# Kernel optimization log

Hardware: AMD Instinct MI355X
Metric: run time of the kernel (lower is better)

Reference implementation:

```python
import jax, jax.numpy as jnp
import numpy as np

B, S, D = 16, 2048, 64
SCALE = 1.0 / np.sqrt(np.float32(D))  # forward divides by sqrt(embedding_dim=64)


def setup_inputs() -> dict:
    key = jax.random.key(0)
    ks = jax.random.split(key, 7)
    return {
        "x": jax.random.normal(ks[0], (B, S, D), dtype=jnp.float32),
        "Wq": jax.random.normal(ks[1], (D, D), dtype=jnp.float32) * 0.02,
        "bq": jax.random.normal(ks[2], (D,), dtype=jnp.float32) * 0.02,
        "Wk": jax.random.normal(ks[3], (D, D), dtype=jnp.float32) * 0.02,
        "bk": jax.random.normal(ks[4], (D,), dtype=jnp.float32) * 0.02,
        "Wv": jax.random.normal(ks[5], (D, D), dtype=jnp.float32) * 0.02,
        "bv": jax.random.normal(ks[6], (D,), dtype=jnp.float32) * 0.02,
    }


def reference(x, Wq, bq, Wk, bk, Wv, bv):
    # Linear projections (weights stored [in, out], math-equivalent to nn.Linear)
    q = jnp.einsum("bsd,de->bse", x, Wq) + bq
    k = jnp.einsum("bsd,de->bse", x, Wk) + bk
    v = jnp.einsum("bsd,de->bse", x, Wv) + bv
    # Unfused scores: [B, S, S]
    scores = jnp.einsum("bqd,bkd->bqk", q, k) * jnp.float32(SCALE)
    causal = jnp.tril(jnp.ones((S, S), dtype=bool))  # mask[:S,:S]
    scores = jnp.where(causal, scores, jnp.float32(-jnp.inf))
    attn = jax.nn.softmax(scores, axis=-1)
    # dropout is identity in eval mode (reference baseline)
    out = jnp.einsum("bqk,bkd->bqd", attn, v)
    return out
```

## Files before the change

kernel.cpp:

```cpp
#include <hip/hip_runtime.h>

#define NB 16
#define SS 2048
#define DD 64

typedef __attribute__((ext_vector_type(8))) short short8;
typedef __attribute__((ext_vector_type(4))) float f32x4;

#define SCL2E 0.18033688011112042f

#define GLOAD_LDS(g, l) __builtin_amdgcn_global_load_lds( \
    (const __attribute__((address_space(1))) void*)(g),   \
    (__attribute__((address_space(3))) void*)(l), 16, 0, 0)

__device__ __forceinline__ short f2bf(float f) {
  union { float f; unsigned u; } v; v.f = f;
  unsigned r = (v.u + 0x7fffu + ((v.u >> 16) & 1u)) >> 16;
  return (short)r;
}

__device__ __forceinline__ unsigned cvtpk_bf16(float lo, float hi) {
  unsigned r;
  asm("v_cvt_pk_bf16_f32 %0, %1, %2" : "=v"(r) : "v"(lo), "v"(hi));
  return r;
}

__device__ __forceinline__ short8 load_a_frag_f32(const float* p) {
  float4 u = *(const float4*)p;
  float4 w = *(const float4*)(p + 4);
  short8 r;
  r[0] = f2bf(u.x); r[1] = f2bf(u.y); r[2] = f2bf(u.z); r[3] = f2bf(u.w);
  r[4] = f2bf(w.x); r[5] = f2bf(w.y); r[6] = f2bf(w.z); r[7] = f2bf(w.w);
  return r;
}

__global__ __launch_bounds__(768) void proj_kernel(
    const float* __restrict__ x,
    const float* __restrict__ Wq, const float* __restrict__ bq,
    const float* __restrict__ Wk, const float* __restrict__ bk,
    const float* __restrict__ Wv, const float* __restrict__ bv,
    ushort* __restrict__ qo, ushort* __restrict__ ko, ushort* __restrict__ vt)
{
  __shared__ __align__(16) ushort Wt[3][64][72];
  __shared__ __align__(16) ushort Vs[64][68];
  const int t = threadIdx.x;
#pragma unroll
  for (int i = 0; i < 4; ++i) {
    int idx = i * 3072 + t * 4;
    int m = idx >> 12, rem = idx & 4095;
    int kk = rem >> 6, n0 = rem & 63;
    const float* src = (m == 0 ? Wq : (m == 1 ? Wk : Wv));
    float4 w4 = *(const float4*)(src + rem);
    Wt[m][n0 + 0][kk] = (ushort)f2bf(w4.x);
    Wt[m][n0 + 1][kk] = (ushort)f2bf(w4.y);
    Wt[m][n0 + 2][kk] = (ushort)f2bf(w4.z);
    Wt[m][n0 + 3][kk] = (ushort)f2bf(w4.w);
  }
  __syncthreads();

  const int lane = t & 63, w = t >> 6;
  const int l15 = lane & 15, quad = lane >> 4;
  const int mm = w >> 2, rr = w & 3;
  const int g = blockIdx.x * 64 + rr * 16 + l15;

  short8 b0 = load_a_frag_f32(x + (size_t)g * 64 + quad * 8);
  short8 b1 = load_a_frag_f32(x + (size_t)g * 64 + 32 + quad * 8);

  const float* bp = (mm == 0 ? bq : (mm == 1 ? bk : bv));
  ushort* outp = (mm == 0 ? qo : ko);

#pragma unroll
  for (int nt = 0; nt < 4; ++nt) {
    const ushort* ap = &Wt[mm][nt * 16 + l15][quad * 8];
    short8 a0 = *(const short8*)ap;
    short8 a1 = *(const short8*)(ap + 32);
    f32x4 acc = {0.f, 0.f, 0.f, 0.f};
    acc = __builtin_amdgcn_mfma_f32_16x16x32_bf16(a0, b0, acc, 0, 0, 0);
    acc = __builtin_amdgcn_mfma_f32_16x16x32_bf16(a1, b1, acc, 0, 0, 0);
    float4 bb = *(const float4*)(bp + nt * 16 + quad * 4);
    uint2 pk;
    pk.x = cvtpk_bf16(acc[0] + bb.x, acc[1] + bb.y);
    pk.y = cvtpk_bf16(acc[2] + bb.z, acc[3] + bb.w);
    if (mm == 2) {
      *(uint2*)&Vs[rr * 16 + l15][nt * 16 + quad * 4] = pk;
    } else {
      int colb = (nt * 16 + quad * 4) * 2;
      if (mm == 1) colb ^= (g & 7) << 4;
      *(uint2*)((char*)outp + (size_t)g * 128 + colb) = pk;
    }
  }
  __syncthreads();
  if (t < 256) {
    const int batch = blockIdx.x >> 5;
    const int ktile = blockIdx.x & 31;
    const int d = t >> 2, j0 = (t & 3) * 16;
    ushort tmp[16];
#pragma unroll
    for (int j = 0; j < 16; ++j) tmp[j] = Vs[j0 + j][d];
    char* base = (char*)vt + ((size_t)batch * SS * DD + ktile * 4096) * 2 + d * 128;
    const int sw = (d & 7) << 4;
    const int bcol = ((j0 >> 5) << 6) + (((j0 >> 4) & 1) << 3);
#pragma unroll
    for (int jj = 0; jj < 4; ++jj)
      *(uint2*)(base + ((bcol + jj * 16) ^ sw)) = ((uint2*)tmp)[jj];
  }
}

template<bool MASKED>
__device__ __forceinline__ void attn32(
    const f32x4 (&c)[2], float& l_acc, f32x4 (&acc)[4],
    const short8 (&vf)[4], int keybase, int qabs, int quad)
{
  unsigned pk[4];
#pragma unroll
  for (int ct = 0; ct < 2; ++ct) {
    float pe[4];
#pragma unroll
    for (int r = 0; r < 4; ++r) {
      float p = __builtin_amdgcn_exp2f(c[ct][r] * SCL2E);
      if (MASKED && (keybase + ct * 16 + quad * 4 + r > qabs)) p = 0.f;
      pe[r] = p;
      l_acc += p;
    }
    pk[ct * 2 + 0] = cvtpk_bf16(pe[0], pe[1]);
    pk[ct * 2 + 1] = cvtpk_bf16(pe[2], pe[3]);
  }
  int4 w4;
  w4.x = (int)pk[0]; w4.y = (int)pk[1]; w4.z = (int)pk[2]; w4.w = (int)pk[3];
  short8 pa = *(short8*)&w4;
  __builtin_amdgcn_s_setprio(1);
#pragma unroll
  for (int nt = 0; nt < 4; ++nt)
    acc[nt] = __builtin_amdgcn_mfma_f32_16x16x32_bf16(pa, vf[nt], acc[nt], 0, 0, 0);
  __builtin_amdgcn_s_setprio(0);
}

__device__ __forceinline__ void stage_tile(
    char* lds, const ushort* kg, const ushort* vt,
    size_t bbyte, int kt, int seg, int lane)
{
  const char* src = (seg < 2)
      ? (const char*)kg + bbyte + (size_t)kt * 8192 + seg * 4096
      : (const char*)vt + bbyte + (size_t)kt * 8192 + (seg - 2) * 4096;
  char* dst = lds + seg * 4096;
#pragma unroll
  for (int i = 0; i < 4; ++i)
    GLOAD_LDS(src + i * 1024 + lane * 16, dst + i * 1024);
}

__global__ __launch_bounds__(256) void attn_kernel(
    const ushort* __restrict__ qg, const ushort* __restrict__ kg,
    const ushort* __restrict__ vt, float* __restrict__ out)
{
  __shared__ __align__(16) char KV[2][16384];

  const int t = threadIdx.x, bid = blockIdx.x;
  const int batch = (bid & 7) * 2 + ((bid >> 3) & 1);
  const int qt = 63 - (bid >> 4);
  const int q0 = qt * 32;
  const int lane = t & 63, w = t >> 6;
  const int l15 = lane & 15, quad = lane >> 4;
  const int h = w >> 1;
  const int qgi = w & 1;
  const int qrow0 = q0 + qgi * 16;
  const size_t bbase = (size_t)batch * SS * DD;
  const size_t bbyte = bbase * 2;

  const ushort* qp = qg + bbase + (size_t)(qrow0 + l15) * 64 + quad * 8;
  short8 a0 = *(const short8*)qp;
  short8 a1 = *(const short8*)(qp + 32);

  f32x4 acc[4];
  float l = 0.f;
#pragma unroll
  for (int nt = 0; nt < 4; ++nt) acc[nt] = (f32x4){0.f, 0.f, 0.f, 0.f};

  const int ktotal = ((q0 + 31) >> 6) + 1;
  const int qabs = qrow0 + l15;

  stage_tile(&KV[0][0], kg, vt, bbyte, 0, w, lane);
  __syncthreads();

  int cur = 0;
  for (int kt = 0; kt < ktotal; ++kt) {
    if (kt + 1 < ktotal)
      stage_tile(&KV[cur ^ 1][0], kg, vt, bbyte, kt + 1, w, lane);

    const char* Kb = &KV[cur][0];
    const char* Vb = &KV[cur][8192];
    short8 kf0[2], kf1[2], vf[4];
#pragma unroll
    for (int c2 = 0; c2 < 2; ++c2) {
      int row = (2 * h + c2) * 16 + l15;
      int sw = (row & 7) << 4;
      kf0[c2] = *(const short8*)(Kb + row * 128 + ((quad * 16) ^ sw));
      kf1[c2] = *(const short8*)(Kb + row * 128 + ((64 + quad * 16) ^ sw));
    }
#pragma unroll
    for (int nt = 0; nt < 4; ++nt) {
      int drow = nt * 16 + l15;
      int sv = (drow & 7) << 4;
      vf[nt] = *(const short8*)(Vb + drow * 128 + ((h * 64 + quad * 16) ^ sv));
    }

    f32x4 c[2];
    __builtin_amdgcn_s_setprio(1);
#pragma unroll
    for (int c2 = 0; c2 < 2; ++c2) {
      f32x4 z = {0.f, 0.f, 0.f, 0.f};
      c[c2] = __builtin_amdgcn_mfma_f32_16x16x32_bf16(kf0[c2], a0, z, 0, 0, 0);
      c[c2] = __builtin_amdgcn_mfma_f32_16x16x32_bf16(kf1[c2], a1, c[c2], 0, 0, 0);
    }
    __builtin_amdgcn_s_setprio(0);

    const int keybase = kt * 64 + h * 32;
    if (kt == ktotal - 1)
      attn32<true >(c, l, acc, vf, keybase, qabs, quad);
    else
      attn32<false>(c, l, acc, vf, keybase, qabs, quad);

    __syncthreads();
    cur ^= 1;
  }

  l += __shfl_xor(l, 16);
  l += __shfl_xor(l, 32);

  __syncthreads();

  float* S = (float*)&KV[0][qgi * 8192];
  if (h == 1) {
#pragma unroll
    for (int r = 0; r < 4; ++r)
#pragma unroll
      for (int nt = 0; nt < 4; ++nt)
        S[(quad * 4 + r) * 68 + nt * 16 + l15] = acc[nt][r];
    if (lane < 16) S[1088 + lane] = l;
  }
  __syncthreads();
  if (h == 0) {
    float lt = l + S[1088 + l15];
#pragma unroll
    for (int r = 0; r < 4; ++r) {
      float iv = 1.0f / __shfl(lt, quad * 4 + r);
      float* orow = out + bbase + (size_t)(qrow0 + quad * 4 + r) * 64 + l15;
#pragma unroll
      for (int nt = 0; nt < 4; ++nt)
        orow[nt * 16] = (acc[nt][r] + S[(quad * 4 + r) * 68 + nt * 16 + l15]) * iv;
    }
  }
}

extern "C" void kernel_launch(void* const* d_in, const int* in_sizes, int n_in,
                              void* d_out, int out_size, void* d_ws, size_t ws_size,
                              hipStream_t stream) {
  (void)in_sizes; (void)n_in; (void)out_size; (void)ws_size;
  const float* x  = (const float*)d_in[0];
  const float* Wq = (const float*)d_in[1];
  const float* bq = (const float*)d_in[2];
  const float* Wk = (const float*)d_in[3];
  const float* bk = (const float*)d_in[4];
  const float* Wv = (const float*)d_in[5];
  const float* bv = (const float*)d_in[6];
  float* out = (float*)d_out;

  ushort* qws = (ushort*)d_ws;
  ushort* kws = qws + (size_t)NB * SS * DD;
  ushort* vws = kws + (size_t)NB * SS * DD;

  proj_kernel<<<dim3(NB * SS / 64), dim3(768), 0, stream>>>(
      x, Wq, bq, Wk, bk, Wv, bv, qws, kws, vws);
  attn_kernel<<<dim3(NB * (SS / 32)), dim3(256), 0, stream>>>(
      qws, kws, vws, out);
}
```

Before: 99.86 us.

## Fuse projection and attention into one persistent kernel with grid barrier

Replaces the separate projection and attention launches with a single 512-block kernel. Each block first computes Q/K/V projections for 64 rows, then waits at a global atomic grid barrier. It then processes two causal query tiles, paired long and short (63-u and u), so every block gets roughly equal work. This removes the second kernel launch and the tail imbalance of causal tiles. In exchange it needs a memset, a spin barrier that assumes all 512 blocks are co-resident, and fewer threads doing the projection phase.

```diff
diff --git a/kernel.cpp b/kernel.cpp
--- a/kernel.cpp
+++ b/kernel.cpp
@@ -3,6 +3,7 @@
 #define NB 16
 #define SS 2048
 #define DD 64
+#define NBLK 512
 
 typedef __attribute__((ext_vector_type(8))) short short8;
 typedef __attribute__((ext_vector_type(4))) float f32x4;
@@ -32,78 +33,6 @@
   r[0] = f2bf(u.x); r[1] = f2bf(u.y); r[2] = f2bf(u.z); r[3] = f2bf(u.w);
   r[4] = f2bf(w.x); r[5] = f2bf(w.y); r[6] = f2bf(w.z); r[7] = f2bf(w.w);
   return r;
-}
-
-__global__ __launch_bounds__(768) void proj_kernel(
-    const float* __restrict__ x,
-    const float* __restrict__ Wq, const float* __restrict__ bq,
-    const float* __restrict__ Wk, const float* __restrict__ bk,
-    const float* __restrict__ Wv, const float* __restrict__ bv,
-    ushort* __restrict__ qo, ushort* __restrict__ ko, ushort* __restrict__ vt)
-{
-  __shared__ __align__(16) ushort Wt[3][64][72];
-  __shared__ __align__(16) ushort Vs[64][68];
-  const int t = threadIdx.x;
-#pragma unroll
-  for (int i = 0; i < 4; ++i) {
-    int idx = i * 3072 + t * 4;
-    int m = idx >> 12, rem = idx & 4095;
-    int kk = rem >> 6, n0 = rem & 63;
-    const float* src = (m == 0 ? Wq : (m == 1 ? Wk : Wv));
-    float4 w4 = *(const float4*)(src + rem);
-    Wt[m][n0 + 0][kk] = (ushort)f2bf(w4.x);
-    Wt[m][n0 + 1][kk] = (ushort)f2bf(w4.y);
-    Wt[m][n0 + 2][kk] = (ushort)f2bf(w4.z);
-    Wt[m][n0 + 3][kk] = (ushort)f2bf(w4.w);
-  }
-  __syncthreads();
-
-  const int lane = t & 63, w = t >> 6;
-  const int l15 = lane & 15, quad = lane >> 4;
-  const int mm = w >> 2, rr = w & 3;
-  const int g = blockIdx.x * 64 + rr * 16 + l15;
-
-  short8 b0 = load_a_frag_f32(x + (size_t)g * 64 + quad * 8);
-  short8 b1 = load_a_frag_f32(x + (size_t)g * 64 + 32 + quad * 8);
-
-  const float* bp = (mm == 0 ? bq : (mm == 1 ? bk : bv));
-  ushort* outp = (mm == 0 ? qo : ko);
-
-#pragma unroll
-  for (int nt = 0; nt < 4; ++nt) {
-    const ushort* ap = &Wt[mm][nt * 16 + l15][quad * 8];
-    short8 a0 = *(const short8*)ap;
-    short8 a1 = *(const short8*)(ap + 32);
-    f32x4 acc = {0.f, 0.f, 0.f, 0.f};
-    acc = __builtin_amdgcn_mfma_f32_16x16x32_bf16(a0, b0, acc, 0, 0, 0);
-    acc = __builtin_amdgcn_mfma_f32_16x16x32_bf16(a1, b1, acc, 0, 0, 0);
-    float4 bb = *(const float4*)(bp + nt * 16 + quad * 4);
-    uint2 pk;
-    pk.x = cvtpk_bf16(acc[0] + bb.x, acc[1] + bb.y);
-    pk.y = cvtpk_bf16(acc[2] + bb.z, acc[3] + bb.w);
-    if (mm == 2) {
-      *(uint2*)&Vs[rr * 16 + l15][nt * 16 + quad * 4] = pk;
-    } else {
-      int colb = (nt * 16 + quad * 4) * 2;
-      if (mm == 1) colb ^= (g & 7) << 4;
-      *(uint2*)((char*)outp + (size_t)g * 128 + colb) = pk;
-    }
-  }
-  __syncthreads();
-  if (t < 256) {
-    const int batch = blockIdx.x >> 5;
-    const int ktile = blockIdx.x & 31;
-    const int d = t >> 2, j0 = (t & 3) * 16;
-    ushort tmp[16];
-#pragma unroll
-    for (int j = 0; j < 16; ++j) tmp[j] = Vs[j0 + j][d];
-    char* base = (char*)vt + ((size_t)batch * SS * DD + ktile * 4096) * 2 + d * 128;
-    const int sw = (d & 7) << 4;
-    const int bcol = ((j0 >> 5) << 6) + (((j0 >> 4) & 1) << 3);
-#pragma unroll
-    for (int jj = 0; jj < 4; ++jj)
-      *(uint2*)(base + ((bcol + jj * 16) ^ sw)) = ((uint2*)tmp)[jj];
-  }
 }
 
 template<bool MASKED>
@@ -148,105 +77,205 @@
     GLOAD_LDS(src + i * 1024 + lane * 16, dst + i * 1024);
 }
 
-__global__ __launch_bounds__(256) void attn_kernel(
-    const ushort* __restrict__ qg, const ushort* __restrict__ kg,
-    const ushort* __restrict__ vt, float* __restrict__ out)
+template<int M>
+__device__ __forceinline__ void proj_unit(
+    ushort (*Wt)[64][72], ushort (*Vs)[68],
+    const short8& b0, const short8& b1, const float* bp,
+    ushort* outp, int g, int lrow, int l15, int quad)
 {
-  __shared__ __align__(16) char KV[2][16384];
+#pragma unroll
+  for (int nt = 0; nt < 4; ++nt) {
+    short8 a0 = *(const short8*)&Wt[M][nt * 16 + l15][quad * 8];
+    short8 a1 = *(const short8*)&Wt[M][nt * 16 + l15][32 + quad * 8];
+    f32x4 acc = {0.f, 0.f, 0.f, 0.f};
+    acc = __builtin_amdgcn_mfma_f32_16x16x32_bf16(a0, b0, acc, 0, 0, 0);
+    acc = __builtin_amdgcn_mfma_f32_16x16x32_bf16(a1, b1, acc, 0, 0, 0);
+    float4 bb = *(const float4*)(bp + nt * 16 + quad * 4);
+    uint2 pk;
+    pk.x = cvtpk_bf16(acc[0] + bb.x, acc[1] + bb.y);
+    pk.y = cvtpk_bf16(acc[2] + bb.z, acc[3] + bb.w);
+    if (M == 2) {
+      *(uint2*)&Vs[lrow][nt * 16 + quad * 4] = pk;
+    } else if (M == 1) {
+      int colb = ((nt * 16 + quad * 4) * 2) ^ ((g & 7) << 4);
+      *(uint2*)((char*)outp + (size_t)g * 128 + colb) = pk;
+    } else {
+      *(uint2*)(outp + (size_t)g * 64 + nt * 16 + quad * 4) = pk;
+    }
+  }
+}
+
+__global__ __launch_bounds__(256, 2) void fused_kernel(
+    const float* __restrict__ x,
+    const float* __restrict__ Wq, const float* __restrict__ bq,
+    const float* __restrict__ Wk, const float* __restrict__ bk,
+    const float* __restrict__ Wv, const float* __restrict__ bv,
+    ushort* __restrict__ qo, ushort* __restrict__ ko, ushort* __restrict__ vt,
+    float* __restrict__ out, unsigned* __restrict__ bar)
+{
+  __shared__ __align__(16) char SMEM[2][16384];
 
   const int t = threadIdx.x, bid = blockIdx.x;
-  const int batch = (bid & 7) * 2 + ((bid >> 3) & 1);
-  const int qt = 63 - (bid >> 4);
-  const int q0 = qt * 32;
   const int lane = t & 63, w = t >> 6;
   const int l15 = lane & 15, quad = lane >> 4;
-  const int h = w >> 1;
-  const int qgi = w & 1;
-  const int qrow0 = q0 + qgi * 16;
-  const size_t bbase = (size_t)batch * SS * DD;
-  const size_t bbyte = bbase * 2;
-
-  const ushort* qp = qg + bbase + (size_t)(qrow0 + l15) * 64 + quad * 8;
-  short8 a0 = *(const short8*)qp;
-  short8 a1 = *(const short8*)(qp + 32);
-
-  f32x4 acc[4];
-  float l = 0.f;
-#pragma unroll
-  for (int nt = 0; nt < 4; ++nt) acc[nt] = (f32x4){0.f, 0.f, 0.f, 0.f};
-
-  const int ktotal = ((q0 + 31) >> 6) + 1;
-  const int qabs = qrow0 + l15;
-
-  stage_tile(&KV[0][0], kg, vt, bbyte, 0, w, lane);
+
+  {
+    ushort (*Wt)[64][72] = (ushort(*)[64][72])&SMEM[0][0];
+    ushort (*Vs)[68] = (ushort(*)[68])(&SMEM[0][0] + 27648);
+
+    const float* Ws[3] = {Wq, Wk, Wv};
+#pragma unroll
+    for (int m = 0; m < 3; ++m)
+#pragma unroll
+      for (int i = 0; i < 4; ++i) {
+        int idx = i * 1024 + t * 4;
+        int kk = idx >> 6, n0 = idx & 63;
+        float4 w4 = *(const float4*)(Ws[m] + kk * 64 + n0);
+        Wt[m][n0 + 0][kk] = (ushort)f2bf(w4.x);
+        Wt[m][n0 + 1][kk] = (ushort)f2bf(w4.y);
+        Wt[m][n0 + 2][kk] = (ushort)f2bf(w4.z);
+        Wt[m][n0 + 3][kk] = (ushort)f2bf(w4.w);
+      }
+    __syncthreads();
+
+    const int rh = w & 1;
+    const int batch = bid >> 5, kt64 = bid & 31;
+
+    for (int rg = 0; rg < 2; ++rg) {
+      const int g = bid * 64 + rg * 32 + rh * 16 + l15;
+      short8 b0 = load_a_frag_f32(x + (size_t)g * 64 + quad * 8);
+      short8 b1 = load_a_frag_f32(x + (size_t)g * 64 + 32 + quad * 8);
+      const int lrow = rh * 16 + l15;
+
+      if (w < 2) {
+        proj_unit<0>(Wt, Vs, b0, b1, bq, qo, g, lrow, l15, quad);
+        proj_unit<2>(Wt, Vs, b0, b1, bv, qo, g, lrow, l15, quad);
+      } else {
+        proj_unit<1>(Wt, Vs, b0, b1, bk, ko, g, lrow, l15, quad);
+      }
+      __syncthreads();
+
+      if (t < 128) {
+        const int d = t & 63, ct = t >> 6;
+        ushort tmp[16];
+#pragma unroll
+        for (int j = 0; j < 16; ++j) tmp[j] = Vs[ct * 16 + j][d];
+        char* base = (char*)vt + ((size_t)batch * SS * DD + kt64 * 4096) * 2 + d * 128;
+        const int sw = (d & 7) << 4;
+#pragma unroll
+        for (int q4 = 0; q4 < 4; ++q4)
+          *(uint2*)(base + ((rg * 64 + q4 * 16 + ct * 8) ^ sw)) = ((uint2*)tmp)[q4];
+      }
+      __syncthreads();
+    }
+  }
+
+  __threadfence();
+  if (t == 0) {
+    __hip_atomic_fetch_add(bar, 1u, __ATOMIC_ACQ_REL, __HIP_MEMORY_SCOPE_AGENT);
+    while (__hip_atomic_load(bar, __ATOMIC_ACQUIRE, __HIP_MEMORY_SCOPE_AGENT) < NBLK)
+      __builtin_amdgcn_s_sleep(4);
+  }
   __syncthreads();
-
-  int cur = 0;
-  for (int kt = 0; kt < ktotal; ++kt) {
-    if (kt + 1 < ktotal)
-      stage_tile(&KV[cur ^ 1][0], kg, vt, bbyte, kt + 1, w, lane);
-
-    const char* Kb = &KV[cur][0];
-    const char* Vb = &KV[cur][8192];
-    short8 kf0[2], kf1[2], vf[4];
-#pragma unroll
-    for (int c2 = 0; c2 < 2; ++c2) {
-      int row = (2 * h + c2) * 16 + l15;
-      int sw = (row & 7) << 4;
-      kf0[c2] = *(const short8*)(Kb + row * 128 + ((quad * 16) ^ sw));
-      kf1[c2] = *(const short8*)(Kb + row * 128 + ((64 + quad * 16) ^ sw));
-    }
-#pragma unroll
-    for (int nt = 0; nt < 4; ++nt) {
-      int drow = nt * 16 + l15;
-      int sv = (drow & 7) << 4;
-      vf[nt] = *(const short8*)(Vb + drow * 128 + ((h * 64 + quad * 16) ^ sv));
-    }
-
-    f32x4 c[2];
-    __builtin_amdgcn_s_setprio(1);
-#pragma unroll
-    for (int c2 = 0; c2 < 2; ++c2) {
-      f32x4 z = {0.f, 0.f, 0.f, 0.f};
-      c[c2] = __builtin_amdgcn_mfma_f32_16x16x32_bf16(kf0[c2], a0, z, 0, 0, 0);
-      c[c2] = __builtin_amdgcn_mfma_f32_16x16x32_bf16(kf1[c2], a1, c[c2], 0, 0, 0);
-    }
-    __builtin_amdgcn_s_setprio(0);
-
-    const int keybase = kt * 64 + h * 32;
-    if (kt == ktotal - 1)
-      attn32<true >(c, l, acc, vf, keybase, qabs, quad);
-    else
-      attn32<false>(c, l, acc, vf, keybase, qabs, quad);
-
-    __syncthreads();
-    cur ^= 1;
-  }
-
-  l += __shfl_xor(l, 16);
-  l += __shfl_xor(l, 32);
-
-  __syncthreads();
-
-  float* S = (float*)&KV[0][qgi * 8192];
-  if (h == 1) {
-#pragma unroll
-    for (int r = 0; r < 4; ++r)
-#pragma unroll
-      for (int nt = 0; nt < 4; ++nt)
-        S[(quad * 4 + r) * 68 + nt * 16 + l15] = acc[nt][r];
-    if (lane < 16) S[1088 + lane] = l;
-  }
-  __syncthreads();
-  if (h == 0) {
-    float lt = l + S[1088 + l15];
-#pragma unroll
-    for (int r = 0; r < 4; ++r) {
-      float iv = 1.0f / __shfl(lt, quad * 4 + r);
-      float* orow = out + bbase + (size_t)(qrow0 + quad * 4 + r) * 64 + l15;
-#pragma unroll
-      for (int nt = 0; nt < 4; ++nt)
-        orow[nt * 16] = (acc[nt][r] + S[(quad * 4 + r) * 68 + nt * 16 + l15]) * iv;
+  __threadfence();
+
+  {
+    const int batch = (bid & 7) * 2 + ((bid >> 3) & 1);
+    const int u = bid >> 4;
+    const int h = w >> 1;
+    const int qgi = w & 1;
+    const size_t bbase = (size_t)batch * SS * DD;
+    const size_t bbyte = bbase * 2;
+
+#pragma unroll
+    for (int qi = 0; qi < 2; ++qi) {
+      const int qt = qi == 0 ? (63 - u) : u;
+      const int q0 = qt * 32;
+      const int qrow0 = q0 + qgi * 16;
+      const int qabs = qrow0 + l15;
+      const int ktotal = ((q0 + 31) >> 6) + 1;
+
+      const ushort* qp = qo + bbase + (size_t)(qrow0 + l15) * 64 + quad * 8;
+      short8 a0 = *(const short8*)qp;
+      short8 a1 = *(const short8*)(qp + 32);
+
+      f32x4 acc[4];
+      float l = 0.f;
+#pragma unroll
+      for (int nt = 0; nt < 4; ++nt) acc[nt] = (f32x4){0.f, 0.f, 0.f, 0.f};
+
+      __syncthreads();
+      stage_tile(&SMEM[0][0], ko, vt, bbyte, 0, w, lane);
+      __syncthreads();
+
+      int cur = 0;
+      for (int kt = 0; kt < ktotal; ++kt) {
+        if (kt + 1 < ktotal)
+          stage_tile(&SMEM[cur ^ 1][0], ko, vt, bbyte, kt + 1, w, lane);
+
+        const char* Kb = &SMEM[cur][0];
+        const char* Vb = &SMEM[cur][8192];
+        short8 kf0[2], kf1[2], vf[4];
+#pragma unroll
+        for (int c2 = 0; c2 < 2; ++c2) {
+          int row = (2 * h + c2) * 16 + l15;
+          int sw = (row & 7) << 4;
+          kf0[c2] = *(const short8*)(Kb + row * 128 + ((quad * 16) ^ sw));
+          kf1[c2] = *(const short8*)(Kb + row * 128 + ((64 + quad * 16) ^ sw));
+        }
+#pragma unroll
+        for (int nt = 0; nt < 4; ++nt) {
+          int drow = nt * 16 + l15;
+          int sv = (drow & 7) << 4;
+          vf[nt] = *(const short8*)(Vb + drow * 128 + ((h * 64 + quad * 16) ^ sv));
+        }
+
+        f32x4 c[2];
+        __builtin_amdgcn_s_setprio(1);
+#pragma unroll
+        for (int c2 = 0; c2 < 2; ++c2) {
+          f32x4 z = {0.f, 0.f, 0.f, 0.f};
+          c[c2] = __builtin_amdgcn_mfma_f32_16x16x32_bf16(kf0[c2], a0, z, 0, 0, 0);
+          c[c2] = __builtin_amdgcn_mfma_f32_16x16x32_bf16(kf1[c2], a1, c[c2], 0, 0, 0);
+        }
+        __builtin_amdgcn_s_setprio(0);
+
+        const int keybase = kt * 64 + h * 32;
+        if (kt == ktotal - 1)
+          attn32<true >(c, l, acc, vf, keybase, qabs, quad);
+        else
+          attn32<false>(c, l, acc, vf, keybase, qabs, quad);
+
+        __syncthreads();
+        cur ^= 1;
+      }
+
+      l += __shfl_xor(l, 16);
+      l += __shfl_xor(l, 32);
+
+      __syncthreads();
+
+      float* S = (float*)&SMEM[0][qgi * 8192];
+      if (h == 1) {
+#pragma unroll
+        for (int r = 0; r < 4; ++r)
+#pragma unroll
+          for (int nt = 0; nt < 4; ++nt)
+            S[(quad * 4 + r) * 68 + nt * 16 + l15] = acc[nt][r];
+        if (lane < 16) S[1088 + lane] = l;
+      }
+      __syncthreads();
+      if (h == 0) {
+        float lt = l + S[1088 + l15];
+#pragma unroll
+        for (int r = 0; r < 4; ++r) {
+          float iv = 1.0f / __shfl(lt, quad * 4 + r);
+          float* orow = out + bbase + (size_t)(qrow0 + quad * 4 + r) * 64 + l15;
+#pragma unroll
+          for (int nt = 0; nt < 4; ++nt)
+            orow[nt * 16] = (acc[nt][r] + S[(quad * 4 + r) * 68 + nt * 16 + l15]) * iv;
+        }
+      }
     }
   }
 }
@@ -267,9 +296,9 @@
   ushort* qws = (ushort*)d_ws;
   ushort* kws = qws + (size_t)NB * SS * DD;
   ushort* vws = kws + (size_t)NB * SS * DD;
-
-  proj_kernel<<<dim3(NB * SS / 64), dim3(768), 0, stream>>>(
-      x, Wq, bq, Wk, bk, Wv, bv, qws, kws, vws);
-  attn_kernel<<<dim3(NB * (SS / 32)), dim3(256), 0, stream>>>(
-      qws, kws, vws, out);
-}
+  unsigned* bar = (unsigned*)(vws + (size_t)NB * SS * DD);
+
+  hipMemsetAsync(bar, 0, 4, stream);
+  fused_kernel<<<dim3(NBLK), dim3(256), 0, stream>>>(
+      x, Wq, bq, Wk, bk, Wv, bv, qws, kws, vws, out, bar);
+}
```

Result: slower. 235.3 us (+135.7%).
